# Kernel tuning notes

Measured on AMD Instinct MI355X. Metric: run time of the kernel, lower is better.

Reference implementation:

```python
import jax, jax.numpy as jnp
import numpy as np

N_EMBED = 1024
EMBED_DIM = 64
DECAY = 0.99
EPS = 1e-05


def setup_inputs() -> dict:
    key = jax.random.key(0)
    k1, k2 = jax.random.split(key)
    z_e = jax.random.normal(k1, (16, 4096, EMBED_DIM), dtype=jnp.float32)
    # torch init: uniform_(-1/n_embed, 1/n_embed)
    embed = (jax.random.uniform(k2, (N_EMBED, EMBED_DIM), dtype=jnp.float32) * 2.0 - 1.0) / N_EMBED
    cluster_size = jnp.zeros((N_EMBED,), dtype=jnp.float32)
    embed_avg = embed.copy()
    return {"z_e": z_e, "embed": embed, "cluster_size": cluster_size, "embed_avg": embed_avg}


def reference(z_e, embed, cluster_size, embed_avg):
    B, N, E = z_e.shape
    flat = z_e.reshape(-1, E)  # [T, E], T = B*N
    dist = (jnp.sum(flat * flat, axis=1, keepdims=True)
            - 2.0 * flat @ embed.T
            + jnp.sum(embed * embed, axis=1)[None, :])  # [T, K]
    embed_ind = jnp.argmin(dist, axis=1)  # argmax(-dist)
    z_q = embed[embed_ind].reshape(B, N, E)

    # training-mode EMA statistics (scatter-add == one-hot matmul, but memory-efficient)
    onehot_sum = jnp.zeros((N_EMBED,), flat.dtype).at[embed_ind].add(1.0)
    embed_sum = jnp.zeros((N_EMBED, E), flat.dtype).at[embed_ind].add(flat)
    new_cluster_size = DECAY * cluster_size + (1.0 - DECAY) * onehot_sum
    new_embed_avg = DECAY * embed_avg + (1.0 - DECAY) * embed_sum
    n = jnp.sum(new_cluster_size)
    cs = (new_cluster_size + EPS) / (n + N_EMBED * EPS) * n
    new_embed = new_embed_avg / cs[:, None]

    diff = jnp.mean((jax.lax.stop_gradient(z_q) - z_e) ** 2)
    z_q_st = z_e + jax.lax.stop_gradient(z_q - z_e)  # straight-through
    return (z_q_st, diff, embed_ind.reshape(B, N), new_embed, new_cluster_size, new_embed_avg)
```

## Files before the change

kernel.cpp:

```cpp
#include <hip/hip_runtime.h>
#include <math.h>

#define T_TOK 65536
#define K_CODE 1024
#define E_DIM 64
#define DECAYF 0.99f
#define EPSF 1e-5f

#define TT 256
#define HCODE 512
#define QCAP 2048
#define HACC 1.3e-3f

typedef short short8 __attribute__((ext_vector_type(8)));
typedef float f32x16 __attribute__((ext_vector_type(16)));

__device__ __forceinline__ float mul_nf(float a, float b) {
#pragma clang fp contract(off)
    return a * b;
}
__device__ __forceinline__ float add_nf(float a, float b) {
#pragma clang fp contract(off)
    return a + b;
}
__device__ __forceinline__ float sub_nf(float a, float b) {
#pragma clang fp contract(off)
    return a - b;
}

__device__ __forceinline__ float np_sq_row(const float* xrow) {
    const float4* xp = reinterpret_cast<const float4*>(xrow);
    float r[8];
#pragma unroll
    for (int g = 0; g < 8; ++g) {
        float4 va = xp[2 * g], vb = xp[2 * g + 1];
        float e[8] = {va.x, va.y, va.z, va.w, vb.x, vb.y, vb.z, vb.w};
#pragma unroll
        for (int j = 0; j < 8; ++j) {
            if (g == 0) r[j] = mul_nf(e[j], e[j]);
            else        r[j] = add_nf(r[j], mul_nf(e[j], e[j]));
        }
    }
    float s01 = add_nf(r[0], r[1]);
    float s23 = add_nf(r[2], r[3]);
    float s45 = add_nf(r[4], r[5]);
    float s67 = add_nf(r[6], r[7]);
    return add_nf(add_nf(s01, s23), add_nf(s45, s67));
}

__device__ __forceinline__ unsigned f2bf_rne(float f) {
    unsigned u = __float_as_uint(f);
    u += 0x7FFFu + ((u >> 16) & 1u);
    return (u >> 16);
}

__device__ __forceinline__ void exact_key(int t0, int tl, int code, float wn,
                                          const float* __restrict__ z_e,
                                          const float* __restrict__ embed,
                                          const float* xn_s,
                                          unsigned long long* key_s) {
    const float4* xp = reinterpret_cast<const float4*>(z_e + (size_t)(t0 + tl) * E_DIM);
    const float4* wp = reinterpret_cast<const float4*>(embed + (size_t)code * E_DIM);
    float d = 0.f;
#pragma unroll
    for (int m = 0; m < 16; ++m) {
        float4 x4 = xp[m];
        float4 w4 = wp[m];
        d = __builtin_fmaf(x4.x, w4.x, d);
        d = __builtin_fmaf(x4.y, w4.y, d);
        d = __builtin_fmaf(x4.z, w4.z, d);
        d = __builtin_fmaf(x4.w, w4.w, d);
    }
    float dist = add_nf(sub_nf(xn_s[tl], d + d), wn);
    unsigned b = __float_as_uint(dist);
    unsigned mk = (b & 0x80000000u) ? ~b : (b | 0x80000000u);
    atomicMin(key_s + tl, ((unsigned long long)mk << 32) | (unsigned)code);
}


__global__ __launch_bounds__(512) void dist_kernel(const float* __restrict__ z_e,
                                                   const float* __restrict__ embed,
                                                   unsigned long long* __restrict__ keys2) {
    __shared__ unsigned short Ws[HCODE * E_DIM];
    __shared__ float wn_s[HCODE];
    __shared__ float xn_s[TT];
    __shared__ unsigned long long key_s[TT];
    __shared__ unsigned q_s[QCAP];
    __shared__ int qc_s;

    int tid = threadIdx.x;
    int lane = tid & 63;
    int wave = tid >> 6;
    int g = lane >> 5;
    int h = blockIdx.x & 1;
    int t0 = (blockIdx.x >> 1) * TT;
    int kbase = h * HCODE;

    if (tid == 0) qc_s = 0;
    if (tid < TT) {
        key_s[tid] = ~0ull;
        xn_s[tid] = np_sq_row(z_e + (size_t)(t0 + tid) * E_DIM);
    }

    {
        int row = tid;
        const float4* wp =
            reinterpret_cast<const float4*>(embed + (size_t)(kbase + row) * E_DIM);
        uint4* WsQ = reinterpret_cast<uint4*>(Ws);
        float r8[8];
#pragma unroll
        for (int gq = 0; gq < 8; ++gq) {
            float4 va = wp[2 * gq], vb = wp[2 * gq + 1];
            float e[8] = {va.x, va.y, va.z, va.w, vb.x, vb.y, vb.z, vb.w};
#pragma unroll
            for (int j = 0; j < 8; ++j) {
                if (gq == 0) r8[j] = mul_nf(e[j], e[j]);
                else         r8[j] = add_nf(r8[j], mul_nf(e[j], e[j]));
            }
            unsigned p0 = f2bf_rne(e[0]) | (f2bf_rne(e[1]) << 16);
            unsigned p1 = f2bf_rne(e[2]) | (f2bf_rne(e[3]) << 16);
            unsigned p2 = f2bf_rne(e[4]) | (f2bf_rne(e[5]) << 16);
            unsigned p3 = f2bf_rne(e[6]) | (f2bf_rne(e[7]) << 16);
            WsQ[row * 8 + (gq ^ (row & 7))] = make_uint4(p0, p1, p2, p3);
        }
        float s01 = add_nf(r8[0], r8[1]);
        float s23 = add_nf(r8[2], r8[3]);
        float s45 = add_nf(r8[4], r8[5]);
        float s67 = add_nf(r8[6], r8[7]);
        wn_s[row] = add_nf(add_nf(s01, s23), add_nf(s45, s67));
    }

    int arow = wave * 32 + (lane & 31);
    const float* xrow = z_e + (size_t)(t0 + arow) * E_DIM;
    short8 afr[4];
#pragma unroll
    for (int kc = 0; kc < 4; ++kc) {
        int base = kc * 16 + g * 8;
        float4 a = *reinterpret_cast<const float4*>(xrow + base);
        float4 b = *reinterpret_cast<const float4*>(xrow + base + 4);
        afr[kc][0] = (short)f2bf_rne(a.x);
        afr[kc][1] = (short)f2bf_rne(a.y);
        afr[kc][2] = (short)f2bf_rne(a.z);
        afr[kc][3] = (short)f2bf_rne(a.w);
        afr[kc][4] = (short)f2bf_rne(b.x);
        afr[kc][5] = (short)f2bf_rne(b.y);
        afr[kc][6] = (short)f2bf_rne(b.z);
        afr[kc][7] = (short)f2bf_rne(b.w);
    }

    __syncthreads();

    float maxr[16];
#pragma unroll
    for (int r = 0; r < 16; ++r) maxr[r] = -INFINITY;

#pragma unroll 2
    for (int tile = 0; tile < 16; ++tile) {
        int cloc = tile * 32 + (lane & 31);
        f32x16 acc;
#pragma unroll
        for (int i = 0; i < 16; ++i) acc[i] = 0.f;
#pragma unroll
        for (int kc = 0; kc < 4; ++kc) {
            int ps = (2 * kc + g) ^ (cloc & 7);
            short8 bfr = *reinterpret_cast<const short8*>(&Ws[cloc * E_DIM + ps * 8]);
            acc = __builtin_amdgcn_mfma_f32_32x32x16_bf16(afr[kc], bfr, acc, 0, 0, 0);
        }
#pragma unroll
        for (int r = 0; r < 16; ++r) maxr[r] = fmaxf(maxr[r], acc[r]);
    }

#pragma unroll
    for (int off = 1; off < 32; off <<= 1) {
#pragma unroll
        for (int r = 0; r < 16; ++r)
            maxr[r] = fmaxf(maxr[r], __shfl_xor(maxr[r], off, 64));
    }
#pragma unroll
    for (int r = 0; r < 16; ++r) maxr[r] -= HACC;

#pragma unroll 2
    for (int tile = 0; tile < 16; ++tile) {
        int cloc = tile * 32 + (lane & 31);
        f32x16 acc;
#pragma unroll
        for (int i = 0; i < 16; ++i) acc[i] = 0.f;
#pragma unroll
        for (int kc = 0; kc < 4; ++kc) {
            int ps = (2 * kc + g) ^ (cloc & 7);
            short8 bfr = *reinterpret_cast<const short8*>(&Ws[cloc * E_DIM + ps * 8]);
            acc = __builtin_amdgcn_mfma_f32_32x32x16_bf16(afr[kc], bfr, acc, 0, 0, 0);
        }
        float tmax = -INFINITY;
#pragma unroll
        for (int r = 0; r < 16; ++r) tmax = fmaxf(tmax, acc[r] - maxr[r]);
        if (tmax >= 0.f) {
#pragma unroll
            for (int r = 0; r < 16; ++r) {
                if (acc[r] >= maxr[r]) {
                    int row = (r & 3) + 8 * (r >> 2) + 4 * g;
                    int tl = wave * 32 + row;
                    int slot = atomicAdd(&qc_s, 1);
                    if (slot < QCAP)
                        q_s[slot] = ((unsigned)tl << 9) | (unsigned)cloc;
                    else
                        exact_key(t0, tl, kbase + cloc, wn_s[cloc], z_e, embed,
                                  xn_s, key_s);
                }
            }
        }
    }
    __syncthreads();

    int qn = qc_s;
    if (qn > QCAP) qn = QCAP;
    for (int e = tid; e < qn; e += 512) {
        unsigned q = q_s[e];
        int tl = (int)(q >> 9);
        int cloc = (int)(q & 511u);
        exact_key(t0, tl, kbase + cloc, wn_s[cloc], z_e, embed, xn_s, key_s);
    }
    __syncthreads();

    if (tid < TT) keys2[(size_t)(t0 + tid) * 2 + h] = key_s[tid];
}

__global__ __launch_bounds__(256) void combine_kernel(const float* __restrict__ z_e,
                                                      const float* __restrict__ embed,
                                                      const unsigned long long* __restrict__ keys2,
                                                      float* __restrict__ out_zq,
                                                      float* __restrict__ out_ind,
                                                      float* __restrict__ diff_acc,
                                                      float* __restrict__ esum_rep,
                                                      float* __restrict__ onehot_rep,
                                                      int rep_mask) {
    __shared__ int sidx[64];
    __shared__ float sred[4];
    int tid = threadIdx.x;
    int t0 = blockIdx.x * 64;

    if (tid < 64) {
        unsigned long long k0 = keys2[(size_t)(t0 + tid) * 2];
        unsigned long long k1 = keys2[(size_t)(t0 + tid) * 2 + 1];
        unsigned long long kv = k0 < k1 ? k0 : k1;
        int bi = (int)(kv & 0x3FFull);
        sidx[tid] = bi;
        out_ind[t0 + tid] = (float)bi;
    }
    __syncthreads();

    float ds = 0.f;
#pragma unroll
    for (int u = 0; u < 4; ++u) {
        int v = u * 256 + tid;
        int tl = v >> 4;
        int c = v & 15;
        int bi = sidx[tl];
        float4 w4 = *reinterpret_cast<const float4*>(embed + (size_t)bi * E_DIM + c * 4);
        float4 x4 = *reinterpret_cast<const float4*>(z_e + (size_t)(t0 + tl) * E_DIM + c * 4);
        float rx = sub_nf(w4.x, x4.x);
        float ry = sub_nf(w4.y, x4.y);
        float rz = sub_nf(w4.z, x4.z);
        float rw = sub_nf(w4.w, x4.w);
        float4 o;
        o.x = add_nf(x4.x, rx);
        o.y = add_nf(x4.y, ry);
        o.z = add_nf(x4.z, rz);
        o.w = add_nf(x4.w, rw);
        *reinterpret_cast<float4*>(out_zq + (size_t)(t0 + tl) * E_DIM + c * 4) = o;
        ds = __builtin_fmaf(rx, rx, ds);
        ds = __builtin_fmaf(ry, ry, ds);
        ds = __builtin_fmaf(rz, rz, ds);
        ds = __builtin_fmaf(rw, rw, ds);
    }
#pragma unroll
    for (int o = 32; o > 0; o >>= 1) ds += __shfl_down(ds, o, 64);
    if ((tid & 63) == 0) sred[tid >> 6] = ds;
    __syncthreads();
    if (tid == 0) atomicAdd(diff_acc, sred[0] + sred[1] + sred[2] + sred[3]);

    int lane = tid & 63;
    int wv = tid >> 6;
    int rep = blockIdx.x & rep_mask;
    float* esum = esum_rep + (size_t)rep * (K_CODE * E_DIM);
    float* onehot = onehot_rep + (size_t)rep * K_CODE;
#pragma unroll
    for (int j = 0; j < 16; ++j) {
        int tl = wv * 16 + j;
        int bi = sidx[tl];
        float xv = z_e[(size_t)(t0 + tl) * E_DIM + lane];
        atomicAdd(&esum[(size_t)bi * E_DIM + lane], xv);
        if (lane == 0) atomicAdd(&onehot[bi], 1.0f);
    }
}

__global__ __launch_bounds__(256) void finalize_kernel(const float* __restrict__ cluster_size,
                                                       const float* __restrict__ onehot_rep,
                                                       const float* __restrict__ ws_diff,
                                                       const float* __restrict__ embed_avg,
                                                       const float* __restrict__ esum_rep,
                                                       float* __restrict__ out_diff,
                                                       float* __restrict__ out_ncs,
                                                       float* __restrict__ out_ne,
                                                       float* __restrict__ out_nea,
                                                       int nrep) {
    __shared__ float ncs_s[K_CODE];
    __shared__ float red[K_CODE];
    int tid = threadIdx.x;

#pragma unroll
    for (int i = 0; i < 4; ++i) {
        int k = tid + 256 * i;
        float oh = 0.f;
        for (int r = 0; r < nrep; ++r) oh += onehot_rep[(size_t)r * K_CODE + k];
        float ncs = DECAYF * cluster_size[k] + (1.0f - DECAYF) * oh;
        ncs_s[k] = ncs;
        red[k] = ncs;
    }
    __syncthreads();
    for (int s = 512; s > 0; s >>= 1) {
        for (int idx = tid; idx < s; idx += 256) red[idx] += red[idx + s];
        __syncthreads();
    }
    float n = red[0];

    if (blockIdx.x == 0) {
#pragma unroll
        for (int i = 0; i < 4; ++i) {
            int k = tid + 256 * i;
            out_ncs[k] = ncs_s[k];
        }
        if (tid == 0) out_diff[0] = ws_diff[0] * (1.0f / 4194304.0f);
    }

    int k = blockIdx.x * 16 + (tid >> 4);
    int c = tid & 15;
    float ncs = ncs_s[k];
    float cs = (ncs + EPSF) / (n + (float)K_CODE * EPSF) * n;

    size_t off = (size_t)k * E_DIM + (size_t)c * 4;
    float4 s4 = make_float4(0.f, 0.f, 0.f, 0.f);
    for (int r = 0; r < nrep; ++r) {
        float4 v = *reinterpret_cast<const float4*>(esum_rep + (size_t)r * (K_CODE * E_DIM) + off);
        s4.x += v.x; s4.y += v.y; s4.z += v.z; s4.w += v.w;
    }
    float4 a = *reinterpret_cast<const float4*>(embed_avg + off);
    float4 nea, ne;
    nea.x = DECAYF * a.x + (1.0f - DECAYF) * s4.x;
    nea.y = DECAYF * a.y + (1.0f - DECAYF) * s4.y;
    nea.z = DECAYF * a.z + (1.0f - DECAYF) * s4.z;
    nea.w = DECAYF * a.w + (1.0f - DECAYF) * s4.w;
    ne.x = nea.x / cs; ne.y = nea.y / cs; ne.z = nea.z / cs; ne.w = nea.w / cs;
    *reinterpret_cast<float4*>(out_nea + off) = nea;
    *reinterpret_cast<float4*>(out_ne + off) = ne;
}

extern "C" void kernel_launch(void* const* d_in, const int* in_sizes, int n_in,
                              void* d_out, int out_size, void* d_ws, size_t ws_size,
                              hipStream_t stream) {
    const float* z_e = (const float*)d_in[0];
    const float* embed = (const float*)d_in[1];
    const float* cluster_size = (const float*)d_in[2];
    const float* embed_avg = (const float*)d_in[3];

    float* out = (float*)d_out;
    float* o_zq = out;
    float* o_diff = out + 4194304;
    float* o_ind = out + 4194305;
    float* o_ne = out + 4194305 + 65536;
    float* o_ncs = o_ne + 65536;
    float* o_nea = o_ncs + 1024;

    float* ws = (float*)d_ws;
    float* ws_diff = ws + 0;
    float* ws_onehot = ws + 16;

    int nrep = 1;
    while (nrep < 8 &&
           (size_t)(8208 + (size_t)(2 * nrep) * 65536 + 262144) * sizeof(float) <= ws_size)
        nrep *= 2;

    float* ws_esum = ws + 8208;
    unsigned long long* ws_keys2 =
        (unsigned long long*)(ws + 8208 + (size_t)nrep * 65536);

    hipMemsetAsync(ws, 0, (size_t)(8208 + (size_t)nrep * 65536) * sizeof(float), stream);

    dist_kernel<<<(T_TOK / TT) * 2, 512, 0, stream>>>(z_e, embed, ws_keys2);
    combine_kernel<<<T_TOK / 64, 256, 0, stream>>>(z_e, embed, ws_keys2, o_zq, o_ind,
                                                   ws_diff, ws_esum, ws_onehot, nrep - 1);
    finalize_kernel<<<64, 256, 0, stream>>>(cluster_size, ws_onehot, ws_diff, embed_avg,
                                            ws_esum, o_diff, o_ncs, o_ne, o_nea, nrep);
}
```

Measured before the change: 193.7 us.

## Fuse combine stage into dist kernel via last-block-done atomic handoff

Removes the separate combine kernel. Each pair of code-half blocks merges its per-token argmin keys into a global array with atomicMax on inverted keys. The second block to finish each token tile, detected through a per-tile counter, then writes z_q, the indices, diff and the EMA scatter-adds. This saves one launch and the keys round trip. In exchange the epilogue runs on only half the blocks after they finish, adds fences and atomics, and the memset grows to cover the keys and flags.

Result: slower. 309.9 us (+60.0%).

```diff
diff --git a/kernel.cpp b/kernel.cpp
--- a/kernel.cpp
+++ b/kernel.cpp
@@ -80,13 +80,22 @@
 
 __global__ __launch_bounds__(512) void dist_kernel(const float* __restrict__ z_e,
                                                    const float* __restrict__ embed,
-                                                   unsigned long long* __restrict__ keys2) {
+                                                   float* __restrict__ out_zq,
+                                                   float* __restrict__ out_ind,
+                                                   float* __restrict__ diff_acc,
+                                                   float* __restrict__ esum_rep,
+                                                   float* __restrict__ onehot_rep,
+                                                   unsigned long long* __restrict__ keys_g,
+                                                   int* __restrict__ flags,
+                                                   int rep_mask) {
     __shared__ unsigned short Ws[HCODE * E_DIM];
     __shared__ float wn_s[HCODE];
     __shared__ float xn_s[TT];
     __shared__ unsigned long long key_s[TT];
     __shared__ unsigned q_s[QCAP];
+    __shared__ int bi_s[TT];
     __shared__ int qc_s;
+    __shared__ int last_s;
 
     int tid = threadIdx.x;
     int lane = tid & 63;
@@ -222,76 +231,42 @@
     }
     __syncthreads();
 
-    if (tid < TT) keys2[(size_t)(t0 + tid) * 2 + h] = key_s[tid];
-}
-
-__global__ __launch_bounds__(256) void combine_kernel(const float* __restrict__ z_e,
-                                                      const float* __restrict__ embed,
-                                                      const unsigned long long* __restrict__ keys2,
-                                                      float* __restrict__ out_zq,
-                                                      float* __restrict__ out_ind,
-                                                      float* __restrict__ diff_acc,
-                                                      float* __restrict__ esum_rep,
-                                                      float* __restrict__ onehot_rep,
-                                                      int rep_mask) {
-    __shared__ int sidx[64];
-    __shared__ float sred[4];
-    int tid = threadIdx.x;
-    int t0 = blockIdx.x * 64;
-
-    if (tid < 64) {
-        unsigned long long k0 = keys2[(size_t)(t0 + tid) * 2];
-        unsigned long long k1 = keys2[(size_t)(t0 + tid) * 2 + 1];
-        unsigned long long kv = k0 < k1 ? k0 : k1;
-        int bi = (int)(kv & 0x3FFull);
-        sidx[tid] = bi;
+    if (tid < TT) atomicMax(&keys_g[t0 + tid], ~key_s[tid]);
+    __threadfence();
+    __syncthreads();
+    if (tid == 0) last_s = atomicAdd(&flags[blockIdx.x >> 1], 1);
+    __syncthreads();
+    if (last_s == 0) return;
+    __threadfence();
+
+    if (tid < TT) {
+        unsigned long long v = atomicMax(&keys_g[t0 + tid], 0ull);
+        int bi = (int)((~v) & 1023ull);
+        bi_s[tid] = bi;
         out_ind[t0 + tid] = (float)bi;
     }
     __syncthreads();
 
-    float ds = 0.f;
-#pragma unroll
-    for (int u = 0; u < 4; ++u) {
-        int v = u * 256 + tid;
-        int tl = v >> 4;
-        int c = v & 15;
-        int bi = sidx[tl];
-        float4 w4 = *reinterpret_cast<const float4*>(embed + (size_t)bi * E_DIM + c * 4);
-        float4 x4 = *reinterpret_cast<const float4*>(z_e + (size_t)(t0 + tl) * E_DIM + c * 4);
-        float rx = sub_nf(w4.x, x4.x);
-        float ry = sub_nf(w4.y, x4.y);
-        float rz = sub_nf(w4.z, x4.z);
-        float rw = sub_nf(w4.w, x4.w);
-        float4 o;
-        o.x = add_nf(x4.x, rx);
-        o.y = add_nf(x4.y, ry);
-        o.z = add_nf(x4.z, rz);
-        o.w = add_nf(x4.w, rw);
-        *reinterpret_cast<float4*>(out_zq + (size_t)(t0 + tl) * E_DIM + c * 4) = o;
-        ds = __builtin_fmaf(rx, rx, ds);
-        ds = __builtin_fmaf(ry, ry, ds);
-        ds = __builtin_fmaf(rz, rz, ds);
-        ds = __builtin_fmaf(rw, rw, ds);
-    }
-#pragma unroll
-    for (int o = 32; o > 0; o >>= 1) ds += __shfl_down(ds, o, 64);
-    if ((tid & 63) == 0) sred[tid >> 6] = ds;
-    __syncthreads();
-    if (tid == 0) atomicAdd(diff_acc, sred[0] + sred[1] + sred[2] + sred[3]);
-
-    int lane = tid & 63;
-    int wv = tid >> 6;
     int rep = blockIdx.x & rep_mask;
     float* esum = esum_rep + (size_t)rep * (K_CODE * E_DIM);
     float* onehot = onehot_rep + (size_t)rep * K_CODE;
-#pragma unroll
-    for (int j = 0; j < 16; ++j) {
-        int tl = wv * 16 + j;
-        int bi = sidx[tl];
+
+    float ds = 0.f;
+#pragma unroll 4
+    for (int it = 0; it < 32; ++it) {
+        int tl = wave * 32 + it;
+        int bi = bi_s[tl];
         float xv = z_e[(size_t)(t0 + tl) * E_DIM + lane];
+        float wv = embed[(size_t)bi * E_DIM + lane];
+        float rr = sub_nf(wv, xv);
+        out_zq[(size_t)(t0 + tl) * E_DIM + lane] = add_nf(xv, rr);
+        ds = __builtin_fmaf(rr, rr, ds);
         atomicAdd(&esum[(size_t)bi * E_DIM + lane], xv);
         if (lane == 0) atomicAdd(&onehot[bi], 1.0f);
     }
+#pragma unroll
+    for (int o = 32; o > 0; o >>= 1) ds += __shfl_down(ds, o, 64);
+    if (lane == 0) atomicAdd(diff_acc, ds);
 }
 
 __global__ __launch_bounds__(256) void finalize_kernel(const float* __restrict__ cluster_size,
@@ -373,22 +348,25 @@
 
     float* ws = (float*)d_ws;
     float* ws_diff = ws + 0;
-    float* ws_onehot = ws + 16;
+    int* ws_flags = (int*)(ws + 16);
+    float* ws_onehot = ws + 512;
 
     int nrep = 1;
     while (nrep < 8 &&
-           (size_t)(8208 + (size_t)(2 * nrep) * 65536 + 262144) * sizeof(float) <= ws_size)
+           (size_t)(8704 + (size_t)(2 * nrep) * 65536 + 131072) * sizeof(float) <= ws_size)
         nrep *= 2;
 
-    float* ws_esum = ws + 8208;
-    unsigned long long* ws_keys2 =
-        (unsigned long long*)(ws + 8208 + (size_t)nrep * 65536);
-
-    hipMemsetAsync(ws, 0, (size_t)(8208 + (size_t)nrep * 65536) * sizeof(float), stream);
-
-    dist_kernel<<<(T_TOK / TT) * 2, 512, 0, stream>>>(z_e, embed, ws_keys2);
-    combine_kernel<<<T_TOK / 64, 256, 0, stream>>>(z_e, embed, ws_keys2, o_zq, o_ind,
-                                                   ws_diff, ws_esum, ws_onehot, nrep - 1);
+    float* ws_esum = ws + 8704;
+    unsigned long long* ws_keys =
+        (unsigned long long*)(ws + 8704 + (size_t)nrep * 65536);
+
+    hipMemsetAsync(ws, 0,
+                   (size_t)(8704 + (size_t)nrep * 65536 + 131072) * sizeof(float),
+                   stream);
+
+    dist_kernel<<<(T_TOK / TT) * 2, 512, 0, stream>>>(z_e, embed, o_zq, o_ind,
+                                                      ws_diff, ws_esum, ws_onehot,
+                                                      ws_keys, ws_flags, nrep - 1);
     finalize_kernel<<<64, 256, 0, stream>>>(cluster_size, ws_onehot, ws_diff, embed_avg,
                                             ws_esum, o_diff, o_ncs, o_ne, o_nea, nrep);
 }
```
